# Kernel tuning notes

Measured on AMD Instinct MI355X. Metric: run time of the kernel, lower is better.

Reference implementation:

```python
import jax, jax.numpy as jnp
import numpy as np

N_DIS = 25000   # disease nodes: indices [0, 25000)
N_MIR = 25000   # mirna nodes:  indices [25000, 50000)
N = N_DIS + N_MIR
E = 600000
EMB = 128
HID = 128


def setup_inputs() -> dict:
    key = jax.random.key(0)
    ks = jax.random.split(key, 14)
    d_features = jax.random.normal(ks[0], (N_DIS, 383), jnp.float32)
    m_features = jax.random.normal(ks[1], (N_MIR, 495), jnp.float32)
    src = jax.random.randint(ks[2], (E,), 0, N, jnp.int32)
    dst = jax.random.randint(ks[3], (E,), 0, N, jnp.int32)
    def lin(k, fan_in, fan_out):
        lim = 1.0 / np.sqrt(fan_in)
        return jax.random.uniform(k, (fan_in, fan_out), jnp.float32, -lim, lim)
    return {
        "d_features": d_features,
        "m_features": m_features,
        "src": src,
        "dst": dst,
        "W_d": lin(ks[4], 383, EMB), "b_d": jnp.zeros((EMB,), jnp.float32),
        "W_m": lin(ks[5], 495, EMB), "b_m": jnp.zeros((EMB,), jnp.float32),
        "W_self1": lin(ks[6], EMB, HID), "W_neigh1": lin(ks[7], EMB, HID),
        "b1": jnp.zeros((HID,), jnp.float32),
        "W_self2": lin(ks[8], HID, HID), "W_neigh2": lin(ks[9], HID, HID),
        "b2": jnp.zeros((HID,), jnp.float32),
    }


def reference(d_features, m_features, src, dst,
              W_d, b_d, W_m, b_m,
              W_self1, W_neigh1, b1, W_self2, W_neigh2, b2):
    # Per-type embedding projection (torch.no_grad in original; dropout eval=identity)
    h_d = d_features @ W_d + b_d            # [N_DIS, EMB]
    h_m = m_features @ W_m + b_m            # [N_MIR, EMB]
    h = jnp.concatenate([h_d, h_m], axis=0)  # [N, EMB]

    # in-degree for mean aggregation (isolated nodes -> mean 0, like DGL fn.mean)
    deg = jax.ops.segment_sum(jnp.ones(src.shape, h.dtype), dst, num_segments=N)
    inv_deg = 1.0 / jnp.maximum(deg, 1.0)    # [N]

    def sage(x, W_self, W_neigh, b):
        # gather src feats, segment-mean into dst, then combine (DGL SAGEConv 'mean')
        agg = jax.ops.segment_sum(x[src], dst, num_segments=N) * inv_deg[:, None]
        return x @ W_self + agg @ W_neigh + b

    h = jax.nn.relu(sage(h, W_self1, W_neigh1, b1))
    h = sage(h, W_self2, W_neigh2, b2)
    return h
```

## Files before the change

kernel.cpp:

```cpp
#include <hip/hip_runtime.h>

#define N_DIS 25000
#define N_MIR 25000
#define NN    50000
#define E_NUM 600000
#define EMB   128

typedef __attribute__((ext_vector_type(8))) short short8v;
typedef __attribute__((ext_vector_type(4))) float floatx4;

typedef const unsigned int __attribute__((address_space(1))) as1_u32;
typedef unsigned int __attribute__((address_space(3))) as3_u32;

__device__ __forceinline__ void gld16(const void* g, void* lds) {
    __builtin_amdgcn_global_load_lds((as1_u32*)g, (as3_u32*)lds, 16, 0, 0);
}

__device__ __forceinline__ floatx4 mfma_bf16_16x16x32(short8v a, short8v b, floatx4 c) {
    asm("v_mfma_f32_16x16x32_bf16 %0, %1, %2, %0" : "+v"(c) : "v"(a), "v"(b));
    return c;
}

__device__ __forceinline__ float us2f(unsigned short u) {
    return __uint_as_float(((unsigned)u) << 16);
}
__device__ __forceinline__ unsigned short f2us(float f) {
    unsigned u = __float_as_uint(f);
    unsigned r = ((u >> 16) & 1u) + 0x7FFFu;
    u += r;
    return (unsigned short)(u >> 16);
}
__device__ __forceinline__ float loadf(const void* p, size_t i, bool isbf) {
    if (isbf) return us2f(((const unsigned short*)p)[i]);
    return ((const float*)p)[i];
}

__global__ __launch_bounds__(256) void gs_zero(int* counts, int* flags) {
    int i = blockIdx.x * blockDim.x + threadIdx.x;
    if (i < NN) counts[i] = 0;
    if (i < 8) flags[i] = 0;
}

__global__ __launch_bounds__(64) void gs_setflag(int* flags, int v) {
    if (threadIdx.x == 0) flags[0] = v;
}

__global__ __launch_bounds__(256) void gs_probe(const void* x, int* flags) {
    const unsigned* u = (const unsigned*)x;
    unsigned w = u[threadIdx.x];
    int e = (int)((w >> 7) & 0xFF);
    if (e >= 118 && e <= 135) atomicAdd(&flags[0], 1);
}

__global__ __launch_bounds__(256) void gs_prepw(const void* Wd, const void* Wm,
                                                const void* Ws1, const void* Wn1,
                                                const void* Ws2, const void* Wn2,
                                                const int* flags, unsigned short* wt) {
    const bool isbf = flags[0] > 128;
    const int t = threadIdx.x;
    const int w = blockIdx.x >> 2;
    const int cq = (blockIdx.x & 3) * 32;
    const void* W;
    unsigned short* oh;
    unsigned short* ol;
    int K, Kp;
    if (w == 0)      { W = Wd;  oh = wt + 0;      ol = wt + 49152;  K = 383; Kp = 384; }
    else if (w == 1) { W = Wm;  oh = wt + 98304;  ol = wt + 163840; K = 495; Kp = 512; }
    else if (w == 2) { W = Ws1; oh = wt + 229376; ol = wt + 245760; K = 128; Kp = 128; }
    else if (w == 3) { W = Wn1; oh = wt + 262144; ol = wt + 278528; K = 128; Kp = 128; }
    else if (w == 4) { W = Ws2; oh = wt + 294912; ol = wt + 311296; K = 128; Kp = 128; }
    else             { W = Wn2; oh = wt + 327680; ol = wt + 344064; K = 128; Kp = 128; }
    for (int c = cq; c < cq + 32; ++c) {
        for (int k = t; k < Kp; k += 256) {
            float x = (k < K) ? loadf(W, (size_t)k * EMB + c, isbf) : 0.f;
            unsigned short h = f2us(x);
            oh[(size_t)c * Kp + k] = h;
            ol[(size_t)c * Kp + k] = f2us(x - us2f(h));
        }
    }
}

__global__ __launch_bounds__(256) void gs_count(const int* dst, int* counts) {
    int e = blockIdx.x * blockDim.x + threadIdx.x;
    if (e < E_NUM) {
        unsigned d = (unsigned)dst[e];
        if (d < (unsigned)NN) atomicAdd(&counts[d], 1);
    }
}

__global__ __launch_bounds__(256) void gs_scan1(const int* counts, int* row_start, int* bsums) {
    __shared__ int tsum[256];
    const int t = threadIdx.x;
    const int base = blockIdx.x * 1024 + t * 4;
    int v0 = (base + 0 < NN) ? counts[base + 0] : 0;
    int v1 = (base + 1 < NN) ? counts[base + 1] : 0;
    int v2 = (base + 2 < NN) ? counts[base + 2] : 0;
    int v3 = (base + 3 < NN) ? counts[base + 3] : 0;
    int s = v0 + v1 + v2 + v3;
    tsum[t] = s;
    __syncthreads();
    for (int off = 1; off < 256; off <<= 1) {
        int xv = 0;
        if (t >= off) xv = tsum[t - off];
        __syncthreads();
        tsum[t] += xv;
        __syncthreads();
    }
    int excl = tsum[t] - s;
    if (base + 0 < NN) row_start[base + 0] = excl;
    excl += v0;
    if (base + 1 < NN) row_start[base + 1] = excl;
    excl += v1;
    if (base + 2 < NN) row_start[base + 2] = excl;
    excl += v2;
    if (base + 3 < NN) row_start[base + 3] = excl;
    if (t == 255) bsums[blockIdx.x] = tsum[255];
}

__global__ __launch_bounds__(64) void gs_scan2(int* bsums, int* row_start, int nb) {
    if (threadIdx.x == 0) {
        int run = 0;
        for (int i = 0; i < nb; ++i) {
            int v = bsums[i];
            bsums[i] = run;
            run += v;
        }
        row_start[NN] = run;
    }
}

__global__ __launch_bounds__(256) void gs_scan3(int* row_start, int* cursor, const int* bsums) {
    const int t = threadIdx.x;
    const int base = blockIdx.x * 1024 + t * 4;
    const int add = bsums[blockIdx.x];
    for (int i = 0; i < 4; ++i) {
        int idx = base + i;
        if (idx < NN) {
            int v = row_start[idx] + add;
            row_start[idx] = v;
            cursor[idx] = v;
        }
    }
}

__global__ __launch_bounds__(256) void gs_scatter(const int* src, const int* dst, int* cursor,
                                                  int* eidx) {
    int e = blockIdx.x * blockDim.x + threadIdx.x;
    if (e < E_NUM) {
        unsigned d = (unsigned)dst[e];
        unsigned sv = (unsigned)src[e];
        if (d < (unsigned)NN && sv < (unsigned)NN) {
            int p = atomicAdd(&cursor[d], 1);
            eidx[p] = (int)sv;
        }
    }
}

__global__ __launch_bounds__(256) void gs_agg(const float* __restrict__ x,
                                              const int* __restrict__ row_start,
                                              const int* __restrict__ eidx,
                                              float* __restrict__ agg) {
    const int t = threadIdx.x;
    const int row = blockIdx.x * 8 + (t >> 5);
    const int tc = (t & 31) * 4;
    if (row >= NN) return;
    const int s0 = row_start[row];
    const int s1 = row_start[row + 1];
    float a0x = 0.f, a0y = 0.f, a0z = 0.f, a0w = 0.f;
    float a1x = 0.f, a1y = 0.f, a1z = 0.f, a1w = 0.f;
    int e = s0;
    for (; e + 1 < s1; e += 2) {
        int sa = eidx[e];
        int sb = eidx[e + 1];
        float4 va = *(const float4*)&x[(size_t)sa * EMB + tc];
        float4 vb = *(const float4*)&x[(size_t)sb * EMB + tc];
        a0x += va.x; a0y += va.y; a0z += va.z; a0w += va.w;
        a1x += vb.x; a1y += vb.y; a1z += vb.z; a1w += vb.w;
    }
    if (e < s1) {
        int sa = eidx[e];
        float4 va = *(const float4*)&x[(size_t)sa * EMB + tc];
        a0x += va.x; a0y += va.y; a0z += va.z; a0w += va.w;
    }
    float inv = (s1 > s0) ? 1.f / (float)(s1 - s0) : 0.f;
    float4 o;
    o.x = (a0x + a1x) * inv;
    o.y = (a0y + a1y) * inv;
    o.z = (a0z + a1z) * inv;
    o.w = (a0w + a1w) * inv;
    *(float4*)&agg[(size_t)row * EMB + tc] = o;
}

__global__ __launch_bounds__(256, 3) void gs_mm(
    const void* __restrict__ Xa, int Ka, const unsigned short* __restrict__ WAh,
    const unsigned short* __restrict__ WAl, int KpA, const void* __restrict__ ba,
    const void* __restrict__ Xb, int Kb, const unsigned short* __restrict__ WBh,
    const unsigned short* __restrict__ WBl, int KpB, const void* __restrict__ bb,
    int splitB, int Ma, int Mb,
    const float* __restrict__ X2, const unsigned short* __restrict__ W2h,
    const unsigned short* __restrict__ W2l,
    const int* __restrict__ flags, float* __restrict__ out, int x1_dyn, int do_relu) {
    __shared__ __align__(16) unsigned char sm[49152];
    unsigned char* smXH = sm;
    unsigned char* smXL = sm + 8192;
    unsigned char* smWH = sm + 16384;
    unsigned char* smWL = sm + 32768;
    const bool isbf = flags[0] > 128;
    const int t = threadIdx.x;
    const bool sideB = (int)blockIdx.x >= splitB;
    const void* X1 = sideB ? Xb : Xa;
    const unsigned short* W1h = sideB ? WBh : WAh;
    const unsigned short* W1l = sideB ? WBl : WAl;
    const int K1 = sideB ? Kb : Ka;
    const int Kp1 = sideB ? KpB : KpA;
    const void* bias = sideB ? bb : ba;
    const int M = sideB ? Mb : Ma;
    const int r0 = (sideB ? ((int)blockIdx.x - splitB) : (int)blockIdx.x) * 64;
    float* outb = out + (sideB ? (size_t)Ma * EMB : 0);
    const bool x1bf = (x1_dyn != 0) && isbf;

    const int l = t & 63;
    const int wv = t >> 6;
    const int wr = wv >> 1, wc = wv & 1;
    const int lr = l & 15, lg = l >> 4;

    floatx4 acc[2][4];
#pragma unroll
    for (int rt = 0; rt < 2; ++rt)
#pragma unroll
        for (int ct = 0; ct < 4; ++ct) acc[rt][ct] = (floatx4){0.f, 0.f, 0.f, 0.f};

    const int nch1 = (K1 + 63) >> 6;
    const int totch = nch1 + (X2 ? 2 : 0);

    const int srX = t >> 2;
    const int skX = (t & 3) << 4;

    for (int ch = 0; ch < totch; ++ch) {
        const void* cX;
        const unsigned short* cWh;
        const unsigned short* cWl;
        int ck0, cK, cKp;
        bool cxbf;
        if (ch < nch1) {
            cX = X1; cWh = W1h; cWl = W1l; ck0 = ch << 6; cK = K1; cKp = Kp1; cxbf = x1bf;
        } else {
            cX = (const void*)X2; cWh = W2h; cWl = W2l;
            ck0 = (ch - nch1) << 6; cK = 128; cKp = 128; cxbf = false;
        }
        const bool cvec = (!cxbf) && (cK == 128);

        __syncthreads();

#pragma unroll
        for (int i = 0; i < 4; ++i) {
            const int p = (wv << 12) + (i << 10) + (l << 4);
            const int col = p >> 7;
            const int g16 = p & 0x7F;
            const size_t so = ((size_t)col * cKp + ck0) * 2 + (size_t)(g16 ^ ((col & 7) << 4));
            gld16((const unsigned char*)cWh + so, smWH + (wv << 12) + (i << 10));
            if (!isbf) gld16((const unsigned char*)cWl + so, smWL + (wv << 12) + (i << 10));
        }

        {
            const int gr = r0 + srX;
            unsigned xu[16];
            if (cvec) {
                if (gr < M) {
                    const float* p = &((const float*)cX)[(size_t)gr * 128 + ck0 + skX];
#pragma unroll
                    for (int q = 0; q < 4; ++q) {
                        float4 v = *(const float4*)(p + (q << 2));
                        xu[q * 4 + 0] = __float_as_uint(v.x);
                        xu[q * 4 + 1] = __float_as_uint(v.y);
                        xu[q * 4 + 2] = __float_as_uint(v.z);
                        xu[q * 4 + 3] = __float_as_uint(v.w);
                    }
                } else {
#pragma unroll
                    for (int j = 0; j < 16; ++j) xu[j] = 0u;
                }
            } else {
#pragma unroll
                for (int j = 0; j < 16; ++j) {
                    int gk = ck0 + skX + j;
                    unsigned v = 0u;
                    if (gr < M && gk < cK)
                        v = cxbf ? (unsigned)((const unsigned short*)cX)[(size_t)gr * cK + gk]
                                 : ((const unsigned*)cX)[(size_t)gr * cK + gk];
                    xu[j] = v;
                }
            }
            const int rowoff = srX << 7;
            const int swz = (srX & 7) << 4;
#pragma unroll
            for (int g = 0; g < 2; ++g) {
                short8v vh, vl;
#pragma unroll
                for (int e = 0; e < 8; ++e) {
                    unsigned u = xu[(g << 3) + e];
                    if (cxbf) {
                        vh[e] = (short)u;
                        vl[e] = 0;
                    } else {
                        unsigned short h = (unsigned short)(u >> 16);
                        vh[e] = (short)h;
                        vl[e] = (short)f2us(__uint_as_float(u) - us2f(h));
                    }
                }
                const int off = rowoff + ((((skX << 1) + (g << 4))) ^ swz);
                *(short8v*)(smXH + off) = vh;
                if (!cxbf) *(short8v*)(smXL + off) = vl;
            }
        }
        __syncthreads();

        const bool skip_xl = cxbf;
        const bool skip_wl = isbf;
#pragma unroll
        for (int ks = 0; ks < 2; ++ks) {
            const int kbyte = (ks << 6) + (lg << 4);
            short8v ah[2], al[2];
#pragma unroll
            for (int rt = 0; rt < 2; ++rt) {
                const int row = wr * 32 + rt * 16 + lr;
                const int off = (row << 7) + (kbyte ^ ((row & 7) << 4));
                ah[rt] = *(const short8v*)(smXH + off);
                if (!skip_xl) al[rt] = *(const short8v*)(smXL + off);
            }
#pragma unroll
            for (int ct = 0; ct < 4; ++ct) {
                const int col = wc * 64 + ct * 16 + lr;
                const int boff = (col << 7) + (kbyte ^ ((col & 7) << 4));
                short8v bh = *(const short8v*)(smWH + boff);
                acc[0][ct] = mfma_bf16_16x16x32(ah[0], bh, acc[0][ct]);
                acc[1][ct] = mfma_bf16_16x16x32(ah[1], bh, acc[1][ct]);
                if (!skip_xl) {
                    acc[0][ct] = mfma_bf16_16x16x32(al[0], bh, acc[0][ct]);
                    acc[1][ct] = mfma_bf16_16x16x32(al[1], bh, acc[1][ct]);
                }
                if (!skip_wl) {
                    short8v bl = *(const short8v*)(smWL + boff);
                    acc[0][ct] = mfma_bf16_16x16x32(ah[0], bl, acc[0][ct]);
                    acc[1][ct] = mfma_bf16_16x16x32(ah[1], bl, acc[1][ct]);
                }
            }
        }
    }

#pragma unroll
    for (int ct = 0; ct < 4; ++ct) {
        const int col = wc * 64 + ct * 16 + lr;
        const float bbv = loadf(bias, col, isbf);
#pragma unroll
        for (int rt = 0; rt < 2; ++rt) {
#pragma unroll
            for (int rr = 0; rr < 4; ++rr) {
                const int row = r0 + wr * 32 + rt * 16 + (lg << 2) + rr;
                if (row < M) {
                    float v = acc[rt][ct][rr] + bbv;
                    if (do_relu) v = v > 0.f ? v : 0.f;
                    outb[(size_t)row * EMB + col] = v;
                }
            }
        }
    }
}

extern "C" __attribute__((visibility("default"))) void kernel_launch(
    void* const* d_in, const int* in_sizes, int n_in, void* d_out, int out_size, void* d_ws,
    size_t ws_size, hipStream_t stream) {
    int iDF = 0, iMF = 1, iSRC = 2, iDST = 3, iWD = 4, iBD = 5, iWM = 6, iBM = 7;
    int iWS1 = 8, iWN1 = 9, iB1 = 10, iWS2 = 11, iWN2 = 12, iB2 = 13;
    long u0 = in_sizes ? (long)in_sizes[0] : 9575000L;
    int dt = -1;
    if (u0 == 49024L || u0 == 98048L || u0 == 196096L) {
        iWD = 0; iWM = 1; iWN1 = 2; iWN2 = 3; iWS1 = 4; iWS2 = 5;
        iB1 = 6; iB2 = 7; iBD = 8; iBM = 9; iDF = 10; iDST = 11; iMF = 12; iSRC = 13;
        if (u0 == 98048L) dt = 1;
        else if (u0 == 196096L) dt = 0;
    } else {
        if (u0 == 19150000L) dt = 1;
        else if (u0 == 38300000L) dt = 0;
    }
    const void* d_features = d_in[iDF];
    const void* m_features = d_in[iMF];
    const int* src = (const int*)d_in[iSRC];
    const int* dst = (const int*)d_in[iDST];
    const void* W_d = d_in[iWD];
    const void* b_d = d_in[iBD];
    const void* W_m = d_in[iWM];
    const void* b_m = d_in[iBM];
    const void* W_self1 = d_in[iWS1];
    const void* W_neigh1 = d_in[iWN1];
    const void* b1 = d_in[iB1];
    const void* W_self2 = d_in[iWS2];
    const void* W_neigh2 = d_in[iWN2];
    const void* b2v = d_in[iB2];

    char* w = (char*)d_ws;
    int* flags = (int*)(w + 0);
    int* counts = (int*)(w + 64);
    int* row_start = (int*)(w + 200064);
    int* cursor = (int*)(w + 400128);
    int* bsums = (int*)(w + 600128);
    int* eidx = (int*)(w + 600384);
    unsigned short* wt = (unsigned short*)(w + 3000448);
    unsigned short* wt_hd = wt + 0;
    unsigned short* wt_ld = wt + 49152;
    unsigned short* wt_hm = wt + 98304;
    unsigned short* wt_lm = wt + 163840;
    unsigned short* wt_hs1 = wt + 229376;
    unsigned short* wt_ls1 = wt + 245760;
    unsigned short* wt_hn1 = wt + 262144;
    unsigned short* wt_ln1 = wt + 278528;
    unsigned short* wt_hs2 = wt + 294912;
    unsigned short* wt_ls2 = wt + 311296;
    unsigned short* wt_hn2 = wt + 327680;
    unsigned short* wt_ln2 = wt + 344064;
    float* hF = (float*)(w + 3721344);
    float* h1F = (float*)(w + 29321344);

    const int NB_SCAN = (NN + 1023) / 1024;
    const int EB = (E_NUM + 255) / 256;
    const int ZB = (NN + 255) / 256;

    hipLaunchKernelGGL(gs_zero, dim3(ZB), dim3(256), 0, stream, counts, flags);
    if (dt == 1)
        hipLaunchKernelGGL(gs_setflag, dim3(1), dim3(64), 0, stream, flags, 1000);
    else if (dt == 0)
        hipLaunchKernelGGL(gs_setflag, dim3(1), dim3(64), 0, stream, flags, 0);
    else
        hipLaunchKernelGGL(gs_probe, dim3(1), dim3(256), 0, stream, d_features, flags);

    hipLaunchKernelGGL(gs_prepw, dim3(24), dim3(256), 0, stream, W_d, W_m, W_self1, W_neigh1,
                       W_self2, W_neigh2, flags, wt);

    hipLaunchKernelGGL(gs_count, dim3(EB), dim3(256), 0, stream, dst, counts);
    hipLaunchKernelGGL(gs_scan1, dim3(NB_SCAN), dim3(256), 0, stream, counts, row_start, bsums);
    hipLaunchKernelGGL(gs_scan2, dim3(1), dim3(64), 0, stream, bsums, row_start, NB_SCAN);
    hipLaunchKernelGGL(gs_scan3, dim3(NB_SCAN), dim3(256), 0, stream, row_start, cursor, bsums);
    hipLaunchKernelGGL(gs_scatter, dim3(EB), dim3(256), 0, stream, src, dst, cursor, eidx);

    const int PBd = (N_DIS + 63) / 64;
    hipLaunchKernelGGL(gs_mm, dim3(2 * PBd), dim3(256), 0, stream,
                       d_features, 383, wt_hd, wt_ld, 384, b_d,
                       m_features, 495, wt_hm, wt_lm, 512, b_m,
                       PBd, N_DIS, N_MIR,
                       (const float*)nullptr, (const unsigned short*)nullptr,
                       (const unsigned short*)nullptr,
                       flags, hF, 1, 0);

    const int AB = NN / 8;
    const int GB = (NN + 63) / 64;

    hipLaunchKernelGGL(gs_agg, dim3(AB), dim3(256), 0, stream, hF, row_start, eidx,
                       (float*)d_out);
    hipLaunchKernelGGL(gs_mm, dim3(GB), dim3(256), 0, stream,
                       (const void*)hF, 128, wt_hs1, wt_ls1, 128, b1,
                       (const void*)nullptr, 0, (const unsigned short*)nullptr,
                       (const unsigned short*)nullptr, 0, (const void*)nullptr,
                       GB, NN, 0,
                       (const float*)d_out, wt_hn1, wt_ln1,
                       flags, h1F, 0, 1);

    hipLaunchKernelGGL(gs_agg, dim3(AB), dim3(256), 0, stream, h1F, row_start, eidx, hF);
    hipLaunchKernelGGL(gs_mm, dim3(GB), dim3(256), 0, stream,
                       (const void*)h1F, 128, wt_hs2, wt_ls2, 128, b2v,
                       (const void*)nullptr, 0, (const unsigned short*)nullptr,
                       (const unsigned short*)nullptr, 0, (const void*)nullptr,
                       GB, NN, 0,
                       (const float*)hF, wt_hn2, wt_ln2,
                       flags, (float*)d_out, 0, 0);
}
```

Measured before the change: 447.2 us.

## Store intermediates as split bf16 hi/lo planes and add direct-to-LDS SAGE GEMM

Intermediate activations are now written as pre-split bf16 high and low planes instead of fp32. The aggregation kernel gathers and re-splits these planes, and a new 128-row, 512-thread SAGE GEMM streams both X planes and both weight planes straight into LDS with global_load_lds. This drops the per-tile fp32-to-bf16 split work and the register-staged X loads in the layer GEMMs. The byte volume per element is unchanged (2+2 bytes), and the aggregation does extra conversions plus twice as many load instructions.

```diff
diff --git a/kernel.cpp b/kernel.cpp
--- a/kernel.cpp
+++ b/kernel.cpp
@@ -156,50 +156,61 @@
     }
 }
 
-__global__ __launch_bounds__(256) void gs_agg(const float* __restrict__ x,
-                                              const int* __restrict__ row_start,
-                                              const int* __restrict__ eidx,
-                                              float* __restrict__ agg) {
+__global__ __launch_bounds__(256) void gs_aggp(const unsigned short* __restrict__ xh,
+                                               const unsigned short* __restrict__ xl,
+                                               const int* __restrict__ row_start,
+                                               const int* __restrict__ eidx,
+                                               unsigned short* __restrict__ oh,
+                                               unsigned short* __restrict__ ol) {
     const int t = threadIdx.x;
     const int row = blockIdx.x * 8 + (t >> 5);
-    const int tc = (t & 31) * 4;
+    const int c4 = (t & 31) * 4;
     if (row >= NN) return;
     const int s0 = row_start[row];
     const int s1 = row_start[row + 1];
-    float a0x = 0.f, a0y = 0.f, a0z = 0.f, a0w = 0.f;
-    float a1x = 0.f, a1y = 0.f, a1z = 0.f, a1w = 0.f;
+    float a0 = 0.f, a1 = 0.f, a2 = 0.f, a3 = 0.f;
+    float b0 = 0.f, b1 = 0.f, b2 = 0.f, b3 = 0.f;
     int e = s0;
     for (; e + 1 < s1; e += 2) {
         int sa = eidx[e];
         int sb = eidx[e + 1];
-        float4 va = *(const float4*)&x[(size_t)sa * EMB + tc];
-        float4 vb = *(const float4*)&x[(size_t)sb * EMB + tc];
-        a0x += va.x; a0y += va.y; a0z += va.z; a0w += va.w;
-        a1x += vb.x; a1y += vb.y; a1z += vb.z; a1w += vb.w;
+        ushort4 ha = *(const ushort4*)&xh[(size_t)sa * EMB + c4];
+        ushort4 la = *(const ushort4*)&xl[(size_t)sa * EMB + c4];
+        ushort4 hb = *(const ushort4*)&xh[(size_t)sb * EMB + c4];
+        ushort4 lb = *(const ushort4*)&xl[(size_t)sb * EMB + c4];
+        a0 += us2f(ha.x) + us2f(la.x); a1 += us2f(ha.y) + us2f(la.y);
+        a2 += us2f(ha.z) + us2f(la.z); a3 += us2f(ha.w) + us2f(la.w);
+        b0 += us2f(hb.x) + us2f(lb.x); b1 += us2f(hb.y) + us2f(lb.y);
+        b2 += us2f(hb.z) + us2f(lb.z); b3 += us2f(hb.w) + us2f(lb.w);
     }
     if (e < s1) {
         int sa = eidx[e];
-        float4 va = *(const float4*)&x[(size_t)sa * EMB + tc];
-        a0x += va.x; a0y += va.y; a0z += va.z; a0w += va.w;
+        ushort4 ha = *(const ushort4*)&xh[(size_t)sa * EMB + c4];
+        ushort4 la = *(const ushort4*)&xl[(size_t)sa * EMB + c4];
+        a0 += us2f(ha.x) + us2f(la.x); a1 += us2f(ha.y) + us2f(la.y);
+        a2 += us2f(ha.z) + us2f(la.z); a3 += us2f(ha.w) + us2f(la.w);
     }
     float inv = (s1 > s0) ? 1.f / (float)(s1 - s0) : 0.f;
-    float4 o;
-    o.x = (a0x + a1x) * inv;
-    o.y = (a0y + a1y) * inv;
-    o.z = (a0z + a1z) * inv;
-    o.w = (a0w + a1w) * inv;
-    *(float4*)&agg[(size_t)row * EMB + tc] = o;
-}
-
-__global__ __launch_bounds__(256, 3) void gs_mm(
+    float f0 = (a0 + b0) * inv, f1 = (a1 + b1) * inv;
+    float f2 = (a2 + b2) * inv, f3 = (a3 + b3) * inv;
+    ushort4 vh, vl;
+    unsigned short h;
+    h = f2us(f0); vh.x = h; vl.x = f2us(f0 - us2f(h));
+    h = f2us(f1); vh.y = h; vl.y = f2us(f1 - us2f(h));
+    h = f2us(f2); vh.z = h; vl.z = f2us(f2 - us2f(h));
+    h = f2us(f3); vh.w = h; vl.w = f2us(f3 - us2f(h));
+    *(ushort4*)&oh[(size_t)row * EMB + c4] = vh;
+    *(ushort4*)&ol[(size_t)row * EMB + c4] = vl;
+}
+
+__global__ __launch_bounds__(256, 3) void gs_mmp(
     const void* __restrict__ Xa, int Ka, const unsigned short* __restrict__ WAh,
     const unsigned short* __restrict__ WAl, int KpA, const void* __restrict__ ba,
     const void* __restrict__ Xb, int Kb, const unsigned short* __restrict__ WBh,
     const unsigned short* __restrict__ WBl, int KpB, const void* __restrict__ bb,
     int splitB, int Ma, int Mb,
-    const float* __restrict__ X2, const unsigned short* __restrict__ W2h,
-    const unsigned short* __restrict__ W2l,
-    const int* __restrict__ flags, float* __restrict__ out, int x1_dyn, int do_relu) {
+    const int* __restrict__ flags, unsigned short* __restrict__ outH,
+    unsigned short* __restrict__ outL) {
     __shared__ __align__(16) unsigned char sm[49152];
     unsigned char* smXH = sm;
     unsigned char* smXL = sm + 8192;
@@ -216,8 +227,8 @@
     const void* bias = sideB ? bb : ba;
     const int M = sideB ? Mb : Ma;
     const int r0 = (sideB ? ((int)blockIdx.x - splitB) : (int)blockIdx.x) * 64;
-    float* outb = out + (sideB ? (size_t)Ma * EMB : 0);
-    const bool x1bf = (x1_dyn != 0) && isbf;
+    unsigned short* oh = outH + (sideB ? (size_t)Ma * EMB : 0);
+    unsigned short* ol = outL + (sideB ? (size_t)Ma * EMB : 0);
 
     const int l = t & 63;
     const int wv = t >> 6;
@@ -231,65 +242,33 @@
         for (int ct = 0; ct < 4; ++ct) acc[rt][ct] = (floatx4){0.f, 0.f, 0.f, 0.f};
 
     const int nch1 = (K1 + 63) >> 6;
-    const int totch = nch1 + (X2 ? 2 : 0);
-
     const int srX = t >> 2;
     const int skX = (t & 3) << 4;
-
-    for (int ch = 0; ch < totch; ++ch) {
-        const void* cX;
-        const unsigned short* cWh;
-        const unsigned short* cWl;
-        int ck0, cK, cKp;
-        bool cxbf;
-        if (ch < nch1) {
-            cX = X1; cWh = W1h; cWl = W1l; ck0 = ch << 6; cK = K1; cKp = Kp1; cxbf = x1bf;
-        } else {
-            cX = (const void*)X2; cWh = W2h; cWl = W2l;
-            ck0 = (ch - nch1) << 6; cK = 128; cKp = 128; cxbf = false;
-        }
-        const bool cvec = (!cxbf) && (cK == 128);
-
+    const bool xbf = isbf;
+
+    for (int ch = 0; ch < nch1; ++ch) {
+        const int ck0 = ch << 6;
         __syncthreads();
-
 #pragma unroll
         for (int i = 0; i < 4; ++i) {
             const int p = (wv << 12) + (i << 10) + (l << 4);
             const int col = p >> 7;
             const int g16 = p & 0x7F;
-            const size_t so = ((size_t)col * cKp + ck0) * 2 + (size_t)(g16 ^ ((col & 7) << 4));
-            gld16((const unsigned char*)cWh + so, smWH + (wv << 12) + (i << 10));
-            if (!isbf) gld16((const unsigned char*)cWl + so, smWL + (wv << 12) + (i << 10));
-        }
-
+            const size_t so = ((size_t)col * Kp1 + ck0) * 2 + (size_t)(g16 ^ ((col & 7) << 4));
+            gld16((const unsigned char*)W1h + so, smWH + (wv << 12) + (i << 10));
+            if (!isbf) gld16((const unsigned char*)W1l + so, smWL + (wv << 12) + (i << 10));
+        }
         {
             const int gr = r0 + srX;
             unsigned xu[16];
-            if (cvec) {
-                if (gr < M) {
-                    const float* p = &((const float*)cX)[(size_t)gr * 128 + ck0 + skX];
-#pragma unroll
-                    for (int q = 0; q < 4; ++q) {
-                        float4 v = *(const float4*)(p + (q << 2));
-                        xu[q * 4 + 0] = __float_as_uint(v.x);
-                        xu[q * 4 + 1] = __float_as_uint(v.y);
-                        xu[q * 4 + 2] = __float_as_uint(v.z);
-                        xu[q * 4 + 3] = __float_as_uint(v.w);
-                    }
-                } else {
-#pragma unroll
-                    for (int j = 0; j < 16; ++j) xu[j] = 0u;
-                }
-            } else {
-#pragma unroll
-                for (int j = 0; j < 16; ++j) {
-                    int gk = ck0 + skX + j;
-                    unsigned v = 0u;
-                    if (gr < M && gk < cK)
-                        v = cxbf ? (unsigned)((const unsigned short*)cX)[(size_t)gr * cK + gk]
-                                 : ((const unsigned*)cX)[(size_t)gr * cK + gk];
-                    xu[j] = v;
-                }
+#pragma unroll
+            for (int j = 0; j < 16; ++j) {
+                int gk = ck0 + skX + j;
+                unsigned v = 0u;
+                if (gr < M && gk < K1)
+                    v = xbf ? (unsigned)((const unsigned short*)X1)[(size_t)gr * K1 + gk]
+                            : ((const unsigned*)X1)[(size_t)gr * K1 + gk];
+                xu[j] = v;
             }
             const int rowoff = srX << 7;
             const int swz = (srX & 7) << 4;
@@ -299,7 +278,7 @@
 #pragma unroll
                 for (int e = 0; e < 8; ++e) {
                     unsigned u = xu[(g << 3) + e];
-                    if (cxbf) {
+                    if (xbf) {
                         vh[e] = (short)u;
                         vl[e] = 0;
                     } else {
@@ -310,13 +289,10 @@
                 }
                 const int off = rowoff + ((((skX << 1) + (g << 4))) ^ swz);
                 *(short8v*)(smXH + off) = vh;
-                if (!cxbf) *(short8v*)(smXL + off) = vl;
+                if (!xbf) *(short8v*)(smXL + off) = vl;
             }
         }
         __syncthreads();
-
-        const bool skip_xl = cxbf;
-        const bool skip_wl = isbf;
 #pragma unroll
         for (int ks = 0; ks < 2; ++ks) {
             const int kbyte = (ks << 6) + (lg << 4);
@@ -326,7 +302,7 @@
                 const int row = wr * 32 + rt * 16 + lr;
                 const int off = (row << 7) + (kbyte ^ ((row & 7) << 4));
                 ah[rt] = *(const short8v*)(smXH + off);
-                if (!skip_xl) al[rt] = *(const short8v*)(smXL + off);
+                if (!xbf) al[rt] = *(const short8v*)(smXL + off);
             }
 #pragma unroll
             for (int ct = 0; ct < 4; ++ct) {
@@ -335,11 +311,11 @@
                 short8v bh = *(const short8v*)(smWH + boff);
                 acc[0][ct] = mfma_bf16_16x16x32(ah[0], bh, acc[0][ct]);
                 acc[1][ct] = mfma_bf16_16x16x32(ah[1], bh, acc[1][ct]);
-                if (!skip_xl) {
+                if (!xbf) {
                     acc[0][ct] = mfma_bf16_16x16x32(al[0], bh, acc[0][ct]);
                     acc[1][ct] = mfma_bf16_16x16x32(al[1], bh, acc[1][ct]);
                 }
-                if (!skip_wl) {
+                if (!isbf) {
                     short8v bl = *(const short8v*)(smWL + boff);
                     acc[0][ct] = mfma_bf16_16x16x32(ah[0], bl, acc[0][ct]);
                     acc[1][ct] = mfma_bf16_16x16x32(ah[1], bl, acc[1][ct]);
@@ -359,8 +335,120 @@
                 const int row = r0 + wr * 32 + rt * 16 + (lg << 2) + rr;
                 if (row < M) {
                     float v = acc[rt][ct][rr] + bbv;
+                    unsigned short h = f2us(v);
+                    oh[(size_t)row * EMB + col] = h;
+                    ol[(size_t)row * EMB + col] = f2us(v - us2f(h));
+                }
+            }
+        }
+    }
+}
+
+__global__ __launch_bounds__(512, 4) void gs_mml(
+    const unsigned short* __restrict__ X1h, const unsigned short* __restrict__ X1l,
+    const unsigned short* __restrict__ W1h, const unsigned short* __restrict__ W1l,
+    const unsigned short* __restrict__ X2h, const unsigned short* __restrict__ X2l,
+    const unsigned short* __restrict__ W2h, const unsigned short* __restrict__ W2l,
+    const void* __restrict__ bias, const int* __restrict__ flags,
+    float* __restrict__ outf, unsigned short* __restrict__ outh,
+    unsigned short* __restrict__ outl, int do_relu) {
+    __shared__ __align__(16) unsigned char sm[65536];
+    unsigned char* smXH = sm;
+    unsigned char* smXL = sm + 16384;
+    unsigned char* smWH = sm + 32768;
+    unsigned char* smWL = sm + 49152;
+    const bool isbf = flags[0] > 128;
+    const int t = threadIdx.x;
+    const int r0 = (int)blockIdx.x * 128;
+    const int l = t & 63;
+    const int wv = t >> 6;
+    const int wr = wv >> 1, wc = wv & 1;
+    const int lr = l & 15, lg = l >> 4;
+
+    floatx4 acc[2][4];
+#pragma unroll
+    for (int rt = 0; rt < 2; ++rt)
+#pragma unroll
+        for (int ct = 0; ct < 4; ++ct) acc[rt][ct] = (floatx4){0.f, 0.f, 0.f, 0.f};
+
+    const int plane = wv >> 1;
+
+    for (int ch = 0; ch < 4; ++ch) {
+        const unsigned short* xh = (ch < 2) ? X1h : X2h;
+        const unsigned short* xl = (ch < 2) ? X1l : X2l;
+        const unsigned short* wh = (ch < 2) ? W1h : W2h;
+        const unsigned short* wl = (ch < 2) ? W1l : W2l;
+        const int ck0b = (ch & 1) << 7;
+
+        __syncthreads();
+#pragma unroll
+        for (int i = 0; i < 8; ++i) {
+            const int q = ((wv & 1) << 13) + (i << 10) + (l << 4);
+            const int rc = q >> 7;
+            const int g16 = q & 0x7F;
+            const int off = g16 ^ ((rc & 7) << 4);
+            if (plane == 0) {
+                const int gr = (r0 + rc < NN) ? (r0 + rc) : (NN - 1);
+                gld16((const unsigned char*)xh + (size_t)gr * 256 + ck0b + off, smXH + q);
+            } else if (plane == 1) {
+                const int gr = (r0 + rc < NN) ? (r0 + rc) : (NN - 1);
+                gld16((const unsigned char*)xl + (size_t)gr * 256 + ck0b + off, smXL + q);
+            } else if (plane == 2) {
+                gld16((const unsigned char*)wh + (size_t)rc * 256 + ck0b + off, smWH + q);
+            } else if (!isbf) {
+                gld16((const unsigned char*)wl + (size_t)rc * 256 + ck0b + off, smWL + q);
+            }
+        }
+        __syncthreads();
+
+#pragma unroll
+        for (int ks = 0; ks < 2; ++ks) {
+            const int kbyte = (ks << 6) + (lg << 4);
+            short8v ah[2], al[2];
+#pragma unroll
+            for (int rt = 0; rt < 2; ++rt) {
+                const int row = wr * 32 + rt * 16 + lr;
+                const int off = (row << 7) + (kbyte ^ ((row & 7) << 4));
+                ah[rt] = *(const short8v*)(smXH + off);
+                al[rt] = *(const short8v*)(smXL + off);
+            }
+#pragma unroll
+            for (int ct = 0; ct < 4; ++ct) {
+                const int col = wc * 64 + ct * 16 + lr;
+                const int boff = (col << 7) + (kbyte ^ ((col & 7) << 4));
+                short8v bh = *(const short8v*)(smWH + boff);
+                acc[0][ct] = mfma_bf16_16x16x32(ah[0], bh, acc[0][ct]);
+                acc[1][ct] = mfma_bf16_16x16x32(ah[1], bh, acc[1][ct]);
+                acc[0][ct] = mfma_bf16_16x16x32(al[0], bh, acc[0][ct]);
+                acc[1][ct] = mfma_bf16_16x16x32(al[1], bh, acc[1][ct]);
+                if (!isbf) {
+                    short8v bl = *(const short8v*)(smWL + boff);
+                    acc[0][ct] = mfma_bf16_16x16x32(ah[0], bl, acc[0][ct]);
+                    acc[1][ct] = mfma_bf16_16x16x32(ah[1], bl, acc[1][ct]);
+                }
+            }
+        }
+    }
+
+#pragma unroll
+    for (int ct = 0; ct < 4; ++ct) {
+        const int col = wc * 64 + ct * 16 + lr;
+        const float bbv = loadf(bias, col, isbf);
+#pragma unroll
+        for (int rt = 0; rt < 2; ++rt) {
+#pragma unroll
+            for (int rr = 0; rr < 4; ++rr) {
+                const int row = r0 + wr * 32 + rt * 16 + (lg << 2) + rr;
+                if (row < NN) {
+                    float v = acc[rt][ct][rr] + bbv;
                     if (do_relu) v = v > 0.f ? v : 0.f;
-                    outb[(size_t)row * EMB + col] = v;
+                    if (outf) {
+                        outf[(size_t)row * EMB + col] = v;
+                    } else {
+                        unsigned short h = f2us(v);
+                        outh[(size_t)row * EMB + col] = h;
+                        outl[(size_t)row * EMB + col] = f2us(v - us2f(h));
+                    }
                 }
             }
         }
@@ -418,8 +506,14 @@
     unsigned short* wt_ls2 = wt + 311296;
     unsigned short* wt_hn2 = wt + 327680;
     unsigned short* wt_ln2 = wt + 344064;
-    float* hF = (float*)(w + 3721344);
-    float* h1F = (float*)(w + 29321344);
+    unsigned short* hFh = (unsigned short*)(w + 3721344);
+    unsigned short* hFl = (unsigned short*)(w + 16521344);
+    unsigned short* h1Fh = (unsigned short*)(w + 29321344);
+    unsigned short* h1Fl = (unsigned short*)(w + 42121344);
+    unsigned short* ag1h = (unsigned short*)d_out;
+    unsigned short* ag1l = ag1h + 6400000;
+    unsigned short* ag2h = hFh;
+    unsigned short* ag2l = hFl;
 
     const int NB_SCAN = (NN + 1023) / 1024;
     const int EB = (E_NUM + 255) / 256;
@@ -443,33 +537,24 @@
     hipLaunchKernelGGL(gs_scatter, dim3(EB), dim3(256), 0, stream, src, dst, cursor, eidx);
 
     const int PBd = (N_DIS + 63) / 64;
-    hipLaunchKernelGGL(gs_mm, dim3(2 * PBd), dim3(256), 0, stream,
+    hipLaunchKernelGGL(gs_mmp, dim3(2 * PBd), dim3(256), 0, stream,
                        d_features, 383, wt_hd, wt_ld, 384, b_d,
                        m_features, 495, wt_hm, wt_lm, 512, b_m,
-                       PBd, N_DIS, N_MIR,
-                       (const float*)nullptr, (const unsigned short*)nullptr,
-                       (const unsigned short*)nullptr,
-                       flags, hF, 1, 0);
+                       PBd, N_DIS, N_MIR, flags, hFh, hFl);
 
     const int AB = NN / 8;
-    const int GB = (NN + 63) / 64;
-
-    hipLaunchKernelGGL(gs_agg, dim3(AB), dim3(256), 0, stream, hF, row_start, eidx,
-                       (float*)d_out);
-    hipLaunchKernelGGL(gs_mm, dim3(GB), dim3(256), 0, stream,
-                       (const void*)hF, 128, wt_hs1, wt_ls1, 128, b1,
-                       (const void*)nullptr, 0, (const unsigned short*)nullptr,
-                       (const unsigned short*)nullptr, 0, (const void*)nullptr,
-                       GB, NN, 0,
-                       (const float*)d_out, wt_hn1, wt_ln1,
-                       flags, h1F, 0, 1);
-
-    hipLaunchKernelGGL(gs_agg, dim3(AB), dim3(256), 0, stream, h1F, row_start, eidx, hF);
-    hipLaunchKernelGGL(gs_mm, dim3(GB), dim3(256), 0, stream,
-                       (const void*)h1F, 128, wt_hs2, wt_ls2, 128, b2v,
-                       (const void*)nullptr, 0, (const unsigned short*)nullptr,
-                       (const unsigned short*)nullptr, 0, (const void*)nullptr,
-                       GB, NN, 0,
-                       (const float*)hF, wt_hn2, wt_ln2,
-                       flags, (float*)d_out, 0, 0);
-}
+    const int GBL = (NN + 127) / 128;
+
+    hipLaunchKernelGGL(gs_aggp, dim3(AB), dim3(256), 0, stream, hFh, hFl, row_start, eidx,
+                       ag1h, ag1l);
+    hipLaunchKernelGGL(gs_mml, dim3(GBL), dim3(512), 0, stream,
+                       hFh, hFl, wt_hs1, wt_ls1, ag1h, ag1l, wt_hn1, wt_ln1,
+                       b1, flags, (float*)nullptr, h1Fh, h1Fl, 1);
+
+    hipLaunchKernelGGL(gs_aggp, dim3(AB), dim3(256), 0, stream, h1Fh, h1Fl, row_start, eidx,
+                       ag2h, ag2l);
+    hipLaunchKernelGGL(gs_mml, dim3(GBL), dim3(512), 0, stream,
+                       h1Fh, h1Fl, wt_hs2, wt_ls2, ag2h, ag2l, wt_hn2, wt_ln2,
+                       b2v, flags, (float*)d_out, (unsigned short*)nullptr,
+                       (unsigned short*)nullptr, 0);
+}
```

Result: faster. 434.8 us (-2.8%).
